# Kernel optimization log

Measured on AMD Instinct MI355X. Metric: run time of the kernel, lower is better.

Reference implementation:

```python
import jax, jax.numpy as jnp
import numpy as np

D_IN = 1024
D_OUT = 1024
NUM_HEADS = 16
HEAD_DIM = D_OUT // NUM_HEADS


def setup_inputs() -> dict:
    key = jax.random.key(0)
    ks = jax.random.split(key, 6)
    s = 0.02
    x = jax.random.normal(ks[0], (1, 4096, D_IN), dtype=jnp.float32)
    W_q = jax.random.normal(ks[1], (D_IN, D_OUT), dtype=jnp.float32) * s
    W_k = jax.random.normal(ks[2], (D_IN, D_OUT), dtype=jnp.float32) * s
    W_v = jax.random.normal(ks[3], (D_IN, D_OUT), dtype=jnp.float32) * s
    W_o = jax.random.normal(ks[4], (D_OUT, D_OUT), dtype=jnp.float32) * s
    b_o = jnp.zeros((D_OUT,), dtype=jnp.float32)
    return {"x": x, "W_q": W_q, "W_k": W_k, "W_v": W_v, "W_o": W_o, "b_o": b_o}


def reference(x, W_q, W_k, W_v, W_o, b_o):
    b, n, _ = x.shape
    # project and split heads: [b, h, n, d]
    def split_heads(t):
        return t.reshape(b, n, NUM_HEADS, HEAD_DIM).transpose(0, 2, 1, 3)
    q = split_heads(x @ W_q)
    k = split_heads(x @ W_k)
    v = split_heads(x @ W_v)
    scale = 1.0 / jnp.sqrt(jnp.float32(HEAD_DIM))
    scores = jnp.einsum('bhqd,bhkd->bhqk', q, k) * scale  # [b,h,n,n]
    causal = jnp.tril(jnp.ones((n, n), dtype=bool))
    scores = jnp.where(causal, scores, -jnp.inf)
    weights = jax.nn.softmax(scores, axis=-1)
    # dropout rate is 0.0 -> identity
    ctx = jnp.einsum('bhqk,bhkd->bhqd', weights, v)
    ctx = ctx.transpose(0, 2, 1, 3).reshape(b, n, D_OUT)
    return ctx @ W_o + b_o
```

## Files before the change

### kernel.cpp

```cpp
#include <hip/hip_runtime.h>
#include <hip/hip_bf16.h>

typedef __hip_bfloat16 bf16;
typedef __attribute__((ext_vector_type(8))) short short8;
typedef __attribute__((ext_vector_type(4))) short short4v;
typedef __attribute__((ext_vector_type(4))) float floatx4;

#define SEQ 4096
#define DIM 1024
#define NH 16
#define HD 64

__device__ __forceinline__ short f2s(float f) { bf16 t = __float2bfloat16(f); return *(short*)&t; }

__device__ __forceinline__ void gload16(const void* g, void* l) {
    __builtin_amdgcn_global_load_lds(
        (const __attribute__((address_space(1))) void*)g,
        (__attribute__((address_space(3))) void*)l, 16, 0, 0);
}

__device__ __forceinline__ short8 cvt8(float4 a, float4 b) {
    short8 s;
    s[0] = f2s(a.x); s[1] = f2s(a.y); s[2] = f2s(a.z); s[3] = f2s(a.w);
    s[4] = f2s(b.x); s[5] = f2s(b.y); s[6] = f2s(b.z); s[7] = f2s(b.w);
    return s;
}

__global__ __launch_bounds__(256) void transpose_cast_kernel(
    const float* __restrict__ W0, const float* __restrict__ W1,
    const float* __restrict__ W2, const float* __restrict__ W3,
    bf16* __restrict__ Wt_all)
{
    const float* W = blockIdx.z == 0 ? W0 : blockIdx.z == 1 ? W1
                   : blockIdx.z == 2 ? W2 : W3;
    bf16* Wt = Wt_all + (size_t)blockIdx.z * DIM * DIM;

    __shared__ float tile[32][33];
    const int n0 = blockIdx.x * 32, k0 = blockIdx.y * 32;
    const int tr = threadIdx.x >> 5;
    const int tc = threadIdx.x & 31;
#pragma unroll
    for (int i = 0; i < 32; i += 8)
        tile[tr + i][tc] = W[(size_t)(k0 + tr + i) * DIM + n0 + tc];
    __syncthreads();
#pragma unroll
    for (int i = 0; i < 32; i += 8)
        Wt[(size_t)(n0 + tr + i) * DIM + k0 + tc] = __float2bfloat16(tile[tc][tr + i]);
}

#define QBM 128
#define QBN 128
#define QBK 64

__global__ __launch_bounds__(256) void qkv_gemm_kernel(
    const float* __restrict__ A, const bf16* __restrict__ Wt,
    bf16* __restrict__ Qb, bf16* __restrict__ Kb, bf16* __restrict__ Vb)
{
    const int z = blockIdx.z;
    const bf16* Bt = Wt + (size_t)z * DIM * DIM;
    bf16* C = z == 0 ? Qb : (z == 1 ? Kb : Vb);
    const float osc = (z == 0) ? 0.125f : 1.0f;

    __shared__ alignas(16) float Af[QBM][QBK];
    __shared__ alignas(16) short Bs[QBN][QBK];

    const int tid  = threadIdx.x;
    const int wave = tid >> 6, lane = tid & 63;
    const int l15  = lane & 15, quad = lane >> 4;
    const int wm = (wave & 1) * 64;
    const int wn = (wave >> 1) * 64;
    const int bm = blockIdx.y * QBM;
    const int bn = blockIdx.x * QBN;

    const int arow = tid >> 4;
    const int agch = (tid & 15) ^ (arow & 15);
    const float* gA = A + (size_t)(bm + arow) * DIM + agch * 4;
    char* ldsA = (char*)&Af[0][0] + wave * 1024;

    const int brow = tid >> 3;
    const int bgch = (tid & 7) ^ (brow & 7);
    const bf16* gB = Bt + (size_t)(bn + brow) * DIM + bgch * 8;
    char* ldsB = (char*)&Bs[0][0] + wave * 1024;

    floatx4 acc[4][4] = {};

    for (int k0 = 0; k0 < DIM; k0 += QBK) {
        __syncthreads();
#pragma unroll
        for (int c = 0; c < 8; ++c)
            gload16(gA + (size_t)c * 16 * DIM + k0, ldsA + c * 4096);
#pragma unroll
        for (int c = 0; c < 4; ++c)
            gload16(gB + (size_t)c * 32 * DIM + k0, ldsB + c * 4096);
        __syncthreads();

#pragma unroll
        for (int c2 = 0; c2 < 2; ++c2) {
            const int g0 = c2 * 8 + quad * 2;
            const int cb = (c2 * 4 + quad) ^ (l15 & 7);
            short8 afr[4], bfr[4];
#pragma unroll
            for (int i = 0; i < 4; ++i) {
                const int ra = wm + i * 16 + l15;
                float4 f0 = *(const float4*)&Af[ra][(g0 ^ l15) * 4];
                float4 f1 = *(const float4*)&Af[ra][((g0 + 1) ^ l15) * 4];
                afr[i] = cvt8(f0, f1);
                bfr[i] = *(const short8*)&Bs[wn + i * 16 + l15][cb * 8];
            }
#pragma unroll
            for (int mi = 0; mi < 4; ++mi)
#pragma unroll
                for (int ni = 0; ni < 4; ++ni)
                    acc[mi][ni] = __builtin_amdgcn_mfma_f32_16x16x32_bf16(
                        afr[mi], bfr[ni], acc[mi][ni], 0, 0, 0);
        }
    }

#pragma unroll
    for (int mi = 0; mi < 4; ++mi)
#pragma unroll
        for (int r = 0; r < 4; ++r) {
            const int row = bm + wm + mi * 16 + quad * 4 + r;
#pragma unroll
            for (int ni = 0; ni < 4; ++ni) {
                const int col = bn + wn + ni * 16 + l15;
                C[(size_t)row * DIM + col] = __float2bfloat16(acc[mi][ni][r] * osc);
            }
        }
}

__global__ __launch_bounds__(256) void out_gemm_kernel(
    const bf16* __restrict__ A, const bf16* __restrict__ Bt,
    const float* __restrict__ bias, float* __restrict__ C)
{
    __shared__ alignas(16) short Asl[128][64];
    __shared__ alignas(16) short Bsl[64][64];

    const int tid  = threadIdx.x;
    const int wave = tid >> 6, lane = tid & 63;
    const int l15  = lane & 15, quad = lane >> 4;
    const int wm = (wave & 1) * 64;
    const int wn = (wave >> 1) * 32;
    const int bm = blockIdx.y * 128;
    const int bn = blockIdx.x * 64;

    const int srow   = tid >> 3;
    const int gchunk = (tid & 7) ^ (srow & 7);
    const bf16* gA = A  + (size_t)(bm + srow) * DIM + gchunk * 8;
    const bf16* gB = Bt + (size_t)(bn + srow) * DIM + gchunk * 8;
    char* ldsA = (char*)&Asl[0][0] + wave * 1024;
    char* ldsB = (char*)&Bsl[0][0] + wave * 1024;

    floatx4 acc[4][2] = {};

    for (int k0 = 0; k0 < DIM; k0 += 64) {
        __syncthreads();
#pragma unroll
        for (int c = 0; c < 4; ++c)
            gload16(gA + (size_t)c * 32 * DIM + k0, ldsA + c * 4096);
#pragma unroll
        for (int c = 0; c < 2; ++c)
            gload16(gB + (size_t)c * 32 * DIM + k0, ldsB + c * 4096);
        __syncthreads();

#pragma unroll
        for (int c2 = 0; c2 < 2; ++c2) {
            const int cb = (c2 * 4 + quad) ^ (l15 & 7);
            short8 afr[4], bfr[2];
#pragma unroll
            for (int i = 0; i < 4; ++i)
                afr[i] = *(const short8*)&Asl[wm + i * 16 + l15][cb * 8];
#pragma unroll
            for (int i = 0; i < 2; ++i)
                bfr[i] = *(const short8*)&Bsl[wn + i * 16 + l15][cb * 8];
#pragma unroll
            for (int mi = 0; mi < 4; ++mi)
#pragma unroll
                for (int ni = 0; ni < 2; ++ni)
                    acc[mi][ni] = __builtin_amdgcn_mfma_f32_16x16x32_bf16(
                        afr[mi], bfr[ni], acc[mi][ni], 0, 0, 0);
        }
    }

#pragma unroll
    for (int mi = 0; mi < 4; ++mi)
#pragma unroll
        for (int r = 0; r < 4; ++r) {
            const int row = bm + wm + mi * 16 + quad * 4 + r;
#pragma unroll
            for (int ni = 0; ni < 2; ++ni) {
                const int col = bn + wn + ni * 16 + l15;
                C[(size_t)row * DIM + col] = acc[mi][ni][r] + bias[col];
            }
        }
}

#define QT 128
#define KT 64
#define LDT 72

__global__ __launch_bounds__(256) void flash_attn_kernel(
    const bf16* __restrict__ Q, const bf16* __restrict__ K,
    const bf16* __restrict__ V, bf16* ctx)
{
    const int lin  = blockIdx.y * 32 + blockIdx.x;
    const int half = lin >> 8, idx = lin & 255;
    const int qj   = half ? (idx & 31) : 31 - (idx & 31);
    const int h    = (idx >> 5) + 8 * half;
    const int q0   = qj * QT;
    const int nkt  = 2 * qj + 2;

    const int tid  = threadIdx.x;
    const int wave = tid >> 6;
    const int lane = tid & 63;
    const int l15  = lane & 15;
    const int quad = lane >> 4;

    __shared__ alignas(16) short Qs[QT][LDT];
    __shared__ alignas(16) short Ks[2][KT][LDT];
    __shared__ alignas(16) short Vt[2][HD][LDT];
    __shared__ alignas(16) short Ps[4][2][16][LDT];

    {
        const int r = tid >> 1, cb = (tid & 1) * 32;
        const short8* src = (const short8*)(Q + (size_t)(q0 + r) * DIM + h * HD + cb);
#pragma unroll
        for (int i = 0; i < 4; ++i)
            *(short8*)&Qs[r][cb + 8 * i] = src[i];
    }

    const int kr = tid >> 2, kc = (tid & 3) * 16;
    const int vr = (tid & 31) * 2, vd = (tid >> 5) * 8;

    short8 kreg0, kreg1, vreg0, vreg1;
    {
        const short8* kp  = (const short8*)(K + (size_t)kr * DIM + h * HD + kc);
        kreg0 = kp[0]; kreg1 = kp[1];
        const short8* vp0 = (const short8*)(V + (size_t)vr * DIM + h * HD + vd);
        const short8* vp1 = (const short8*)(V + (size_t)(vr + 1) * DIM + h * HD + vd);
        vreg0 = vp0[0]; vreg1 = vp1[0];
    }
    *(short8*)&Ks[0][kr][kc]     = kreg0;
    *(short8*)&Ks[0][kr][kc + 8] = kreg1;
#pragma unroll
    for (int i = 0; i < 8; ++i) {
        unsigned int pv = (unsigned int)(unsigned short)vreg0[i]
                        | ((unsigned int)(unsigned short)vreg1[i] << 16);
        *(unsigned int*)&Vt[0][vd + i][vr] = pv;
    }
    {
        const size_t nb = (size_t)KT;
        const short8* kp  = (const short8*)(K + (nb + kr) * DIM + h * HD + kc);
        kreg0 = kp[0]; kreg1 = kp[1];
        const short8* vp0 = (const short8*)(V + (nb + vr) * DIM + h * HD + vd);
        const short8* vp1 = (const short8*)(V + (nb + vr + 1) * DIM + h * HD + vd);
        vreg0 = vp0[0]; vreg1 = vp1[0];
    }

    __syncthreads();

    short8 qfrag[2][2];
#pragma unroll
    for (int s = 0; s < 2; ++s)
#pragma unroll
        for (int c = 0; c < 2; ++c)
            qfrag[s][c] = *(const short8*)&Qs[wave * 32 + s * 16 + l15][c * 32 + quad * 8];

    short8 onesf;
#pragma unroll
    for (int i = 0; i < 8; ++i) onesf[i] = (short)0x3F80;

    floatx4 o_acc[2][4] = {};
    floatx4 lacc[2] = {};

    for (int kt = 0; kt < nkt; ++kt) {
        const int b = kt & 1;

        floatx4 sT[2][4] = {};
#pragma unroll
        for (int n = 0; n < 4; ++n)
#pragma unroll
            for (int c = 0; c < 2; ++c) {
                short8 kf = *(const short8*)&Ks[b][n * 16 + l15][c * 32 + quad * 8];
#pragma unroll
                for (int s = 0; s < 2; ++s)
                    sT[s][n] = __builtin_amdgcn_mfma_f32_16x16x32_bf16(
                        kf, qfrag[s][c], sT[s][n], 0, 0, 0);
            }

        const int kbase = kt * KT;
        if (kt >= nkt - 2) {
#pragma unroll
            for (int s = 0; s < 2; ++s) {
                const int qrow = q0 + wave * 32 + s * 16 + l15;
#pragma unroll
                for (int n = 0; n < 4; ++n) {
                    const int key0 = kbase + n * 16 + quad * 4;
                    short4v pk;
#pragma unroll
                    for (int r = 0; r < 4; ++r) {
                        float p = (key0 + r <= qrow) ? __expf(sT[s][n][r]) : 0.f;
                        pk[r] = f2s(p);
                    }
                    *(short4v*)&Ps[wave][s][l15][n * 16 + quad * 4] = pk;
                }
            }
        } else {
#pragma unroll
            for (int s = 0; s < 2; ++s)
#pragma unroll
                for (int n = 0; n < 4; ++n) {
                    short4v pk;
#pragma unroll
                    for (int r = 0; r < 4; ++r)
                        pk[r] = f2s(__expf(sT[s][n][r]));
                    *(short4v*)&Ps[wave][s][l15][n * 16 + quad * 4] = pk;
                }
        }

        short8 pfrag[2][2];
#pragma unroll
        for (int s = 0; s < 2; ++s) {
            pfrag[s][0] = *(const short8*)&Ps[wave][s][l15][quad * 8];
            pfrag[s][1] = *(const short8*)&Ps[wave][s][l15][32 + quad * 8];
        }
#pragma unroll
        for (int n = 0; n < 4; ++n)
#pragma unroll
            for (int c = 0; c < 2; ++c) {
                short8 vf = *(const short8*)&Vt[b][n * 16 + l15][c * 32 + quad * 8];
#pragma unroll
                for (int s = 0; s < 2; ++s)
                    o_acc[s][n] = __builtin_amdgcn_mfma_f32_16x16x32_bf16(
                        pfrag[s][c], vf, o_acc[s][n], 0, 0, 0);
            }
#pragma unroll
        for (int s = 0; s < 2; ++s) {
            lacc[s] = __builtin_amdgcn_mfma_f32_16x16x32_bf16(pfrag[s][0], onesf, lacc[s], 0, 0, 0);
            lacc[s] = __builtin_amdgcn_mfma_f32_16x16x32_bf16(pfrag[s][1], onesf, lacc[s], 0, 0, 0);
        }

        if (kt + 1 < nkt) {
            *(short8*)&Ks[b ^ 1][kr][kc]     = kreg0;
            *(short8*)&Ks[b ^ 1][kr][kc + 8] = kreg1;
#pragma unroll
            for (int i = 0; i < 8; ++i) {
                unsigned int pv = (unsigned int)(unsigned short)vreg0[i]
                                | ((unsigned int)(unsigned short)vreg1[i] << 16);
                *(unsigned int*)&Vt[b ^ 1][vd + i][vr] = pv;
            }
            if (kt + 2 < nkt) {
                const size_t nb = (size_t)(kt + 2) * KT;
                const short8* kp  = (const short8*)(K + (nb + kr) * DIM + h * HD + kc);
                kreg0 = kp[0]; kreg1 = kp[1];
                const short8* vp0 = (const short8*)(V + (nb + vr) * DIM + h * HD + vd);
                const short8* vp1 = (const short8*)(V + (nb + vr + 1) * DIM + h * HD + vd);
                vreg0 = vp0[0]; vreg1 = vp1[0];
            }
        }
        __syncthreads();
    }

#pragma unroll
    for (int s = 0; s < 2; ++s)
#pragma unroll
        for (int r = 0; r < 4; ++r) {
            const float inv = 1.0f / lacc[s][r];
            const int row = q0 + wave * 32 + s * 16 + quad * 4 + r;
#pragma unroll
            for (int n = 0; n < 4; ++n)
                ctx[(size_t)row * DIM + h * HD + n * 16 + l15] =
                    __float2bfloat16(o_acc[s][n][r] * inv);
        }
}

extern "C" void kernel_launch(void* const* d_in, const int* in_sizes, int n_in,
                              void* d_out, int out_size, void* d_ws, size_t ws_size,
                              hipStream_t stream)
{
    const float* x  = (const float*)d_in[0];
    const float* Wq = (const float*)d_in[1];
    const float* Wk = (const float*)d_in[2];
    const float* Wv = (const float*)d_in[3];
    const float* Wo = (const float*)d_in[4];
    const float* bo = (const float*)d_in[5];
    float* out = (float*)d_out;

    bf16* Wt_all = (bf16*)d_ws;
    bf16* Qb     = Wt_all + (size_t)4 * DIM * DIM;
    bf16* V      = (bf16*)d_out;
    bf16* Kb     = V + (size_t)SEQ * DIM;
    bf16* ctx    = Qb;
    const bf16* Wot = Wt_all + (size_t)3 * DIM * DIM;

    transpose_cast_kernel<<<dim3(32, 32, 4), 256, 0, stream>>>(Wq, Wk, Wv, Wo, Wt_all);

    qkv_gemm_kernel<<<dim3(DIM / QBN, SEQ / QBM, 3), 256, 0, stream>>>(
        x, Wt_all, Qb, Kb, V);

    flash_attn_kernel<<<dim3(32, NH), 256, 0, stream>>>(Qb, Kb, V, ctx);

    out_gemm_kernel<<<dim3(DIM / 64, SEQ / 128), 256, 0, stream>>>(
        ctx, Wot, bo, out);
}
```

Baseline: 197.6 us.

## Keep P in registers via permuted V layout, use exp2 with folded log2e scale

The attention kernel now builds the P operand for the PV MFMA directly from the score accumulators, with no trip through shared memory. It permutes the key ordering of the transposed V tile (vslot) so the register layout of the score accumulators matches the B-operand layout. Q fragments are loaded straight from global memory into registers, and the Q scale now includes log2(e) so a hardware exp2 can replace expf. The next K/V tile is stored to LDS before the softmax and PV work rather than after it. These changes remove the Ps and Qs LDS round-trips and some transcendental cost, at the price of a subtler layout mapping.

```diff
diff --git a/kernel.cpp b/kernel.cpp
--- a/kernel.cpp
+++ b/kernel.cpp
@@ -3,13 +3,21 @@
 
 typedef __hip_bfloat16 bf16;
 typedef __attribute__((ext_vector_type(8))) short short8;
-typedef __attribute__((ext_vector_type(4))) short short4v;
 typedef __attribute__((ext_vector_type(4))) float floatx4;
 
 #define SEQ 4096
 #define DIM 1024
 #define NH 16
 #define HD 64
+
+#if defined(__has_builtin)
+#if __has_builtin(__builtin_amdgcn_exp2f)
+#define EXP2(x) __builtin_amdgcn_exp2f(x)
+#endif
+#endif
+#ifndef EXP2
+#define EXP2(x) exp2f(x)
+#endif
 
 __device__ __forceinline__ short f2s(float f) { bf16 t = __float2bfloat16(f); return *(short*)&t; }
 
@@ -59,7 +67,7 @@
     const int z = blockIdx.z;
     const bf16* Bt = Wt + (size_t)z * DIM * DIM;
     bf16* C = z == 0 ? Qb : (z == 1 ? Kb : Vb);
-    const float osc = (z == 0) ? 0.125f : 1.0f;
+    const float osc = (z == 0) ? 0.18033688f : 1.0f;
 
     __shared__ alignas(16) float Af[QBM][QBK];
     __shared__ alignas(16) short Bs[QBN][QBK];
@@ -216,21 +224,23 @@
     const int l15  = lane & 15;
     const int quad = lane >> 4;
 
-    __shared__ alignas(16) short Qs[QT][LDT];
     __shared__ alignas(16) short Ks[2][KT][LDT];
     __shared__ alignas(16) short Vt[2][HD][LDT];
-    __shared__ alignas(16) short Ps[4][2][16][LDT];
-
-    {
-        const int r = tid >> 1, cb = (tid & 1) * 32;
-        const short8* src = (const short8*)(Q + (size_t)(q0 + r) * DIM + h * HD + cb);
-#pragma unroll
-        for (int i = 0; i < 4; ++i)
-            *(short8*)&Qs[r][cb + 8 * i] = src[i];
+
+    short8 qfrag[2][2];
+#pragma unroll
+    for (int s = 0; s < 2; ++s) {
+        const bf16* qp = Q + (size_t)(q0 + wave * 32 + s * 16 + l15) * DIM
+                       + h * HD + quad * 8;
+#pragma unroll
+        for (int c = 0; c < 2; ++c)
+            qfrag[s][c] = *(const short8*)(qp + c * 32);
     }
 
     const int kr = tid >> 2, kc = (tid & 3) * 16;
     const int vr = (tid & 31) * 2, vd = (tid >> 5) * 8;
+    const int vslot = ((vr >> 5) & 1) * 32 + ((vr >> 2) & 3) * 8
+                    + ((vr >> 4) & 1) * 4  + ((vr >> 1) & 1) * 2;
 
     short8 kreg0, kreg1, vreg0, vreg1;
     {
@@ -246,7 +256,7 @@
     for (int i = 0; i < 8; ++i) {
         unsigned int pv = (unsigned int)(unsigned short)vreg0[i]
                         | ((unsigned int)(unsigned short)vreg1[i] << 16);
-        *(unsigned int*)&Vt[0][vd + i][vr] = pv;
+        *(unsigned int*)&Vt[0][vd + i][vslot] = pv;
     }
     {
         const size_t nb = (size_t)KT;
@@ -259,13 +269,6 @@
 
     __syncthreads();
 
-    short8 qfrag[2][2];
-#pragma unroll
-    for (int s = 0; s < 2; ++s)
-#pragma unroll
-        for (int c = 0; c < 2; ++c)
-            qfrag[s][c] = *(const short8*)&Qs[wave * 32 + s * 16 + l15][c * 32 + quad * 8];
-
     short8 onesf;
 #pragma unroll
     for (int i = 0; i < 8; ++i) onesf[i] = (short)0x3F80;
@@ -288,58 +291,6 @@
                         kf, qfrag[s][c], sT[s][n], 0, 0, 0);
             }
 
-        const int kbase = kt * KT;
-        if (kt >= nkt - 2) {
-#pragma unroll
-            for (int s = 0; s < 2; ++s) {
-                const int qrow = q0 + wave * 32 + s * 16 + l15;
-#pragma unroll
-                for (int n = 0; n < 4; ++n) {
-                    const int key0 = kbase + n * 16 + quad * 4;
-                    short4v pk;
-#pragma unroll
-                    for (int r = 0; r < 4; ++r) {
-                        float p = (key0 + r <= qrow) ? __expf(sT[s][n][r]) : 0.f;
-                        pk[r] = f2s(p);
-                    }
-                    *(short4v*)&Ps[wave][s][l15][n * 16 + quad * 4] = pk;
-                }
-            }
-        } else {
-#pragma unroll
-            for (int s = 0; s < 2; ++s)
-#pragma unroll
-                for (int n = 0; n < 4; ++n) {
-                    short4v pk;
-#pragma unroll
-                    for (int r = 0; r < 4; ++r)
-                        pk[r] = f2s(__expf(sT[s][n][r]));
-                    *(short4v*)&Ps[wave][s][l15][n * 16 + quad * 4] = pk;
-                }
-        }
-
-        short8 pfrag[2][2];
-#pragma unroll
-        for (int s = 0; s < 2; ++s) {
-            pfrag[s][0] = *(const short8*)&Ps[wave][s][l15][quad * 8];
-            pfrag[s][1] = *(const short8*)&Ps[wave][s][l15][32 + quad * 8];
-        }
-#pragma unroll
-        for (int n = 0; n < 4; ++n)
-#pragma unroll
-            for (int c = 0; c < 2; ++c) {
-                short8 vf = *(const short8*)&Vt[b][n * 16 + l15][c * 32 + quad * 8];
-#pragma unroll
-                for (int s = 0; s < 2; ++s)
-                    o_acc[s][n] = __builtin_amdgcn_mfma_f32_16x16x32_bf16(
-                        pfrag[s][c], vf, o_acc[s][n], 0, 0, 0);
-            }
-#pragma unroll
-        for (int s = 0; s < 2; ++s) {
-            lacc[s] = __builtin_amdgcn_mfma_f32_16x16x32_bf16(pfrag[s][0], onesf, lacc[s], 0, 0, 0);
-            lacc[s] = __builtin_amdgcn_mfma_f32_16x16x32_bf16(pfrag[s][1], onesf, lacc[s], 0, 0, 0);
-        }
-
         if (kt + 1 < nkt) {
             *(short8*)&Ks[b ^ 1][kr][kc]     = kreg0;
             *(short8*)&Ks[b ^ 1][kr][kc + 8] = kreg1;
@@ -347,7 +298,7 @@
             for (int i = 0; i < 8; ++i) {
                 unsigned int pv = (unsigned int)(unsigned short)vreg0[i]
                                 | ((unsigned int)(unsigned short)vreg1[i] << 16);
-                *(unsigned int*)&Vt[b ^ 1][vd + i][vr] = pv;
+                *(unsigned int*)&Vt[b ^ 1][vd + i][vslot] = pv;
             }
             if (kt + 2 < nkt) {
                 const size_t nb = (size_t)(kt + 2) * KT;
@@ -358,6 +309,59 @@
                 vreg0 = vp0[0]; vreg1 = vp1[0];
             }
         }
+
+        short8 pfrag[2][2];
+        const int kbase = kt * KT;
+        if (kt >= nkt - 2) {
+#pragma unroll
+            for (int s = 0; s < 2; ++s) {
+                const int qrow = q0 + wave * 32 + s * 16 + l15;
+                float p[4][4];
+#pragma unroll
+                for (int n = 0; n < 4; ++n) {
+                    const int key0 = kbase + n * 16 + quad * 4;
+#pragma unroll
+                    for (int r = 0; r < 4; ++r)
+                        p[n][r] = (key0 + r <= qrow) ? EXP2(sT[s][n][r]) : 0.f;
+                }
+#pragma unroll
+                for (int c = 0; c < 2; ++c) {
+                    short8 f;
+#pragma unroll
+                    for (int j = 0; j < 8; ++j)
+                        f[j] = f2s(p[c * 2 + (j >> 2)][j & 3]);
+                    pfrag[s][c] = f;
+                }
+            }
+        } else {
+#pragma unroll
+            for (int s = 0; s < 2; ++s)
+#pragma unroll
+                for (int c = 0; c < 2; ++c) {
+                    short8 f;
+#pragma unroll
+                    for (int j = 0; j < 8; ++j)
+                        f[j] = f2s(EXP2(sT[s][c * 2 + (j >> 2)][j & 3]));
+                    pfrag[s][c] = f;
+                }
+        }
+
+#pragma unroll
+        for (int n = 0; n < 4; ++n)
+#pragma unroll
+            for (int c = 0; c < 2; ++c) {
+                short8 vf = *(const short8*)&Vt[b][n * 16 + l15][c * 32 + quad * 8];
+#pragma unroll
+                for (int s = 0; s < 2; ++s)
+                    o_acc[s][n] = __builtin_amdgcn_mfma_f32_16x16x32_bf16(
+                        pfrag[s][c], vf, o_acc[s][n], 0, 0, 0);
+            }
+#pragma unroll
+        for (int s = 0; s < 2; ++s) {
+            lacc[s] = __builtin_amdgcn_mfma_f32_16x16x32_bf16(pfrag[s][0], onesf, lacc[s], 0, 0, 0);
+            lacc[s] = __builtin_amdgcn_mfma_f32_16x16x32_bf16(pfrag[s][1], onesf, lacc[s], 0, 0, 0);
+        }
+
         __syncthreads();
     }
 
```

New measurement: 193.2 us. 2.3% less time.
